# Kernel tuning notes

Measured on AMD Instinct MI355X. Metric: run time of the kernel, lower is better.

## Reference

```python
import jax, jax.numpy as jnp
import numpy as np

# Constants mirroring privacy_config
LEAK = 0.95          # membrane_leak_rate
REFR = 2.0           # refractory_period
SYN_EPS = 0.1        # synaptic_epsilon (threshold noise scale & privacy-cost factor)
NOISE_SCALE = 0.05   # spike_noise_scale on inputs
THRESH = 1.0         # spike_threshold init
SIZES = [1024, 2048, 1024, 512]
T, B = 16, 256


def setup_inputs() -> dict:
    key = jax.random.key(0)
    ks = jax.random.split(key, 16)
    inp = {"inputs": jax.random.normal(ks[0], (B, SIZES[0]), dtype=jnp.float32)}
    for i in range(3):
        nin, nout = SIZES[i], SIZES[i + 1]
        inp[f"w{i}"] = jax.random.normal(ks[1 + i], (nout, nin), dtype=jnp.float32) * 0.1
        inp[f"th{i}"] = jnp.full((nout,), THRESH, dtype=jnp.float32)
        inp[f"cn{i}"] = jax.random.normal(ks[4 + i], (T, B, nout), dtype=jnp.float32)
        inp[f"tn{i}"] = jax.random.normal(ks[7 + i], (T, B, nout), dtype=jnp.float32)
    inp["time_steps"] = T
    return inp


def _forward(inputs, ws, ths, cns, tns):
    # Vectorized leaky integrate-and-fire across (batch, neuron), scanned over time.
    Bsz = inputs.shape[0]
    Tn = cns[0].shape[0]
    nL = len(ws)
    V0 = tuple(jnp.zeros((Bsz, w.shape[0]), inputs.dtype) for w in ws)
    ls0 = tuple(jnp.full((Bsz, w.shape[0]), -1e9, inputs.dtype) for w in ws)  # last spike time
    wnorms = [jnp.linalg.norm(w, axis=1) for w in ws]  # per-neuron weight-vector norm [N]
    times = jnp.arange(1, Tn + 1, dtype=inputs.dtype)

    def step(carry, xs):
        t, cn_t, tn_t = xs
        Vs, ls = carry
        act = inputs  # input is re-presented at each time step (layer_activities[0])
        nV, nls, sps = [], [], []
        for i in range(nL):
            # per-neuron input noise ~ N(0, scale^2) dotted with w -> N(0, scale^2*||w||^2)
            cur = act @ ws[i].T + cn_t[i] * (NOISE_SCALE * wnorms[i])  # [B, N]
            refrac = (t - ls[i]) < REFR  # refractory neurons skip the update entirely
            Vn = jnp.where(refrac, Vs[i], LEAK * Vs[i] + cur)
            thr = ths[i] + tn_t[i] * SYN_EPS  # noisy privacy threshold
            sp = jnp.logical_and(jnp.logical_not(refrac), Vn > thr)
            nV.append(jnp.where(sp, 0.0, Vn))         # reset membrane on spike
            nls.append(jnp.where(sp, t, ls[i]))
            act = sp.astype(inputs.dtype)              # spikes feed next layer
            sps.append(act)
        return (tuple(nV), tuple(nls)), tuple(sps)

    _, spikes = jax.lax.scan(step, (V0, ls0), (times, tuple(cns), tuple(tns)))
    # spikes: tuple of [T, B, N_l] per layer

    # privacy cost: eps * (spikes in trailing 10-step window)/10 * ||w_neuron||, summed over all calls
    idx = jnp.arange(Tn)
    idx_hi = idx + 1
    idx_lo = jnp.clip(idx - 9, 0, Tn)
    cost = jnp.zeros((), inputs.dtype)
    tot = jnp.zeros((), inputs.dtype)
    cnt = 0
    for sp, wn in zip(spikes, wnorms):
        cs = jnp.concatenate([jnp.zeros_like(sp[:1]), jnp.cumsum(sp, axis=0)], axis=0)
        win = cs[idx_hi] - cs[idx_lo]  # [T, B, N] trailing-window spike counts
        cost = cost + SYN_EPS * jnp.sum(win / 10.0 * wn)
        tot = tot + jnp.sum(sp)
        cnt += sp.size
    # network entropy over the binary {0,1} spike pattern values
    p1 = tot / cnt
    p0 = 1.0 - p1
    eps = 1e-12
    entropy = -(p1 * jnp.log2(p1 + eps) + p0 * jnp.log2(p0 + eps))

    out = spikes[-1][-1]  # last layer activity at final time step, [B, N_last]
    return out, cost, entropy


def reference(inputs, w0, w1, w2, th0, th1, th2, cn0, cn1, cn2, tn0, tn1, tn2, time_steps):
    return _forward(inputs, (w0, w1, w2), (th0, th1, th2), (cn0, cn1, cn2), (tn0, tn1, tn2))
```

## Files before the change

### kernel.cpp

```cpp
#include <hip/hip_runtime.h>
#include <math.h>


#define T_STEPS 16

typedef short short8 __attribute__((ext_vector_type(8)));
typedef float floatx4 __attribute__((ext_vector_type(4)));

__device__ inline ushort f2bf(float x) {
  unsigned int u = __float_as_uint(x);
  unsigned int r = (u + 0x7FFFu + ((u >> 16) & 1u)) >> 16;
  return (ushort)r;
}
__device__ inline float bf2f(ushort h) {
  return __uint_as_float(((unsigned int)h) << 16);
}
__device__ inline floatx4 mfma16(short8 a, short8 b, floatx4 c) {
  return __builtin_amdgcn_mfma_f32_16x16x32_bf16(a, b, c, 0, 0, 0);
}

__device__ inline void gload16(const ushort* g, ushort* l) {
  __builtin_amdgcn_global_load_lds(
      (const __attribute__((address_space(1))) void*)g,
      (__attribute__((address_space(3))) void*)l, 16, 0, 0);
}

__device__ inline void stage_split16(const float* __restrict__ src, ushort* dsth, ushort* dstl) {
  float fv[16];
  #pragma unroll
  for (int i = 0; i < 4; ++i) *(float4*)&fv[4 * i] = *(const float4*)(src + 4 * i);
  unsigned int ph[8], pl[8];
  #pragma unroll
  for (int i = 0; i < 8; ++i) {
    ushort h0 = f2bf(fv[2 * i]);
    ushort l0 = f2bf(fv[2 * i] - bf2f(h0));
    ushort h1 = f2bf(fv[2 * i + 1]);
    ushort l1 = f2bf(fv[2 * i + 1] - bf2f(h1));
    ph[i] = (unsigned int)h0 | ((unsigned int)h1 << 16);
    pl[i] = (unsigned int)l0 | ((unsigned int)l1 << 16);
  }
  *(uint4*)dsth       = make_uint4(ph[0], ph[1], ph[2], ph[3]);
  *(uint4*)(dsth + 8) = make_uint4(ph[4], ph[5], ph[6], ph[7]);
  *(uint4*)dstl       = make_uint4(pl[0], pl[1], pl[2], pl[3]);
  *(uint4*)(dstl + 8) = make_uint4(pl[4], pl[5], pl[6], pl[7]);
}

__device__ inline void cost_store_bucket(float csum, int cnt, float2* __restrict__ cbuf,
                                         int bucket_base) {
  #pragma unroll
  for (int off = 32; off > 0; off >>= 1) {
    csum += __shfl_down(csum, off);
    cnt  += __shfl_down(cnt, off);
  }
  __shared__ float sc[4];
  __shared__ int   si[4];
  int wid = threadIdx.x >> 6;
  if ((threadIdx.x & 63) == 0) { sc[wid] = csum; si[wid] = cnt; }
  __syncthreads();
  if (threadIdx.x == 0) {
    float c = sc[0] + sc[1] + sc[2] + sc[3];
    int   k = si[0] + si[1] + si[2] + si[3];
    float2 v;
    v.x = c * 0.01f;
    v.y = (float)k;
    cbuf[bucket_base + blockIdx.x] = v;
  }
}


__global__ __launch_bounds__(256) void setup_kernel(const float* __restrict__ w0,
                                                    const float* __restrict__ w1,
                                                    const float* __restrict__ w2,
                                                    const float* __restrict__ inputs,
                                                    float* __restrict__ wn,
                                                    ushort* __restrict__ w1b,
                                                    ushort* __restrict__ w2b,
                                                    float* __restrict__ base0C) {
  __shared__ ushort Ah[64][72], Al[64][72], Bh[64][72], Bl[64][72];
  const int bid = blockIdx.x;
  const int tid = threadIdx.x;

  if (bid < 896) {
    int r = bid * 4 + (tid >> 6);
    int lane = tid & 63;
    const float* row; int K;
    if (r < 2048)      { row = w0 + (size_t)r * 1024;          K = 1024; }
    else if (r < 3072) { row = w1 + (size_t)(r - 2048) * 2048; K = 2048; }
    else               { row = w2 + (size_t)(r - 3072) * 1024; K = 1024; }
    float ss = 0.f;
    for (int k = lane; k < K; k += 64) { float x = row[k]; ss += x * x; }
    #pragma unroll
    for (int off = 32; off > 0; off >>= 1) ss += __shfl_down(ss, off);
    if (lane == 0) wn[r] = sqrtf(ss);
    return;
  }
  if (bid < 2176) {
    int i = ((bid - 896) * 256 + tid) * 8;
    const float* src; ushort* dst;
    if (i < 2097152) { src = w1 + i; dst = w1b + i; }
    else             { src = w2 + (i - 2097152); dst = w2b + (i - 2097152); }
    float4 a = *(const float4*)src;
    float4 b = *(const float4*)(src + 4);
    unsigned int p0 = (unsigned int)f2bf(a.x) | ((unsigned int)f2bf(a.y) << 16);
    unsigned int p1 = (unsigned int)f2bf(a.z) | ((unsigned int)f2bf(a.w) << 16);
    unsigned int p2 = (unsigned int)f2bf(b.x) | ((unsigned int)f2bf(b.y) << 16);
    unsigned int p3 = (unsigned int)f2bf(b.z) | ((unsigned int)f2bf(b.w) << 16);
    *(uint4*)dst = make_uint4(p0, p1, p2, p3);
    return;
  }

  const int rb = bid - 2176;
  const int m0 = (rb & 3) * 64;
  const int n0 = (rb >> 2) * 64;
  const int lane = tid & 63, wv = tid >> 6;
  const int wm = wv & 1, wn2 = wv >> 1;
  const int l15 = lane & 15, quad = lane >> 4;
  const int sr = tid >> 2, scol = (tid & 3) * 16;

  floatx4 acc[2][2];
  #pragma unroll
  for (int i = 0; i < 2; ++i)
    #pragma unroll
    for (int j = 0; j < 2; ++j) acc[i][j] = (floatx4){0.f, 0.f, 0.f, 0.f};

  for (int k0 = 0; k0 < 1024; k0 += 64) {
    stage_split16(inputs + (size_t)(m0 + sr) * 1024 + k0 + scol, &Ah[sr][scol], &Al[sr][scol]);
    stage_split16(w0 + (size_t)(n0 + sr) * 1024 + k0 + scol, &Bh[sr][scol], &Bl[sr][scol]);
    __syncthreads();
    #pragma unroll
    for (int ks = 0; ks < 2; ++ks) {
      short8 ah[2], al[2], bh[2], bl[2];
      #pragma unroll
      for (int s = 0; s < 2; ++s) {
        ah[s] = *(const short8*)&Ah[32 * wm + 16 * s + l15][ks * 32 + quad * 8];
        al[s] = *(const short8*)&Al[32 * wm + 16 * s + l15][ks * 32 + quad * 8];
        bh[s] = *(const short8*)&Bh[32 * wn2 + 16 * s + l15][ks * 32 + quad * 8];
        bl[s] = *(const short8*)&Bl[32 * wn2 + 16 * s + l15][ks * 32 + quad * 8];
      }
      #pragma unroll
      for (int sm = 0; sm < 2; ++sm)
        #pragma unroll
        for (int sn = 0; sn < 2; ++sn) {
          acc[sm][sn] = mfma16(ah[sm], bh[sn], acc[sm][sn]);
          acc[sm][sn] = mfma16(ah[sm], bl[sn], acc[sm][sn]);
          acc[sm][sn] = mfma16(al[sm], bh[sn], acc[sm][sn]);
        }
    }
    __syncthreads();
  }
  #pragma unroll
  for (int sm = 0; sm < 2; ++sm)
    #pragma unroll
    for (int sn = 0; sn < 2; ++sn)
      #pragma unroll
      for (int r = 0; r < 4; ++r) {
        int m = m0 + 32 * wm + 16 * sm + quad * 4 + r;
        int n = n0 + 32 * wn2 + 16 * sn + l15;
        base0C[(size_t)m * 2048 + n] = acc[sm][sn][r];
      }
}


template<int K, int N, int BM, bool LAST>
__global__ __launch_bounds__(256) void gemm_lif_kernel(const ushort* __restrict__ A,
                                                       const ushort* __restrict__ W,
                                                       const float* __restrict__ cn,
                                                       const float* __restrict__ tn,
                                                       const float* __restrict__ th,
                                                       const float* __restrict__ wnv,
                                                       ushort* __restrict__ spout,
                                                       float* __restrict__ outF,
                                                       float2* __restrict__ cbuf,
                                                       int bucket_base) {
  __shared__ __attribute__((aligned(16))) ushort As[2][BM * 64];
  __shared__ __attribute__((aligned(16))) ushort Bs[2][64 * 64];
  constexpr int NSTEP = K / 64;
  constexpr int NT = N / 64;
  constexpr int MT = 4096 / BM;
  constexpr int NWG = MT * NT;
  constexpr int SM = BM / 32;

  const int orig = ((int)blockIdx.x % 8) * (NWG / 8) + (int)blockIdx.x / 8;
  const int m0 = (orig / NT) * BM;
  const int n0 = (orig % NT) * 64;

  const int tid = threadIdx.x;
  const int lane = tid & 63, wv = tid >> 6;
  const int wm = wv & 1, wn2 = wv >> 1;
  const int l15 = lane & 15, quad = lane >> 4;

  const ushort* Ab = A + (size_t)m0 * K;
  const ushort* Wb = W + (size_t)n0 * K;

  const int lrow = lane >> 3;
  const int lslot = (lane & 7) ^ lrow;

  floatx4 acc[SM][2];
  #pragma unroll
  for (int i = 0; i < SM; ++i)
    #pragma unroll
    for (int j = 0; j < 2; ++j) acc[i][j] = (floatx4){0.f, 0.f, 0.f, 0.f};

  auto stage = [&](int buf, int k0) {
    #pragma unroll
    for (int h = 0; h < SM; ++h) {
      int r0 = wv * (BM / 4) + h * 8;
      gload16(Ab + (size_t)(r0 + lrow) * K + k0 + lslot * 8, &As[buf][r0 * 64]);
    }
    #pragma unroll
    for (int h = 0; h < 2; ++h) {
      int r0 = wv * 16 + h * 8;
      gload16(Wb + (size_t)(r0 + lrow) * K + k0 + lslot * 8, &Bs[buf][r0 * 64]);
    }
  };
  auto compute = [&](int buf) {
    #pragma unroll
    for (int ks = 0; ks < 2; ++ks) {
      short8 af[SM], bf[2];
      #pragma unroll
      for (int s = 0; s < SM; ++s) {
        int arow = wm * (BM / 2) + s * 16 + l15;
        af[s] = *(const short8*)&As[buf][arow * 64 + (((ks * 4 + quad) ^ (arow & 7)) << 3)];
      }
      #pragma unroll
      for (int s = 0; s < 2; ++s) {
        int brow = wn2 * 32 + s * 16 + l15;
        bf[s] = *(const short8*)&Bs[buf][brow * 64 + (((ks * 4 + quad) ^ (brow & 7)) << 3)];
      }
      #pragma unroll
      for (int sm = 0; sm < SM; ++sm)
        #pragma unroll
        for (int sn = 0; sn < 2; ++sn)
          acc[sm][sn] = mfma16(af[sm], bf[sn], acc[sm][sn]);
    }
  };

  stage(0, 0);
  __syncthreads();
  for (int kk = 0; kk < NSTEP; ++kk) {
    int buf = kk & 1;
    if (kk + 1 < NSTEP) stage(buf ^ 1, (kk + 1) * 64);
    compute(buf);
    __syncthreads();
  }

  float csum = 0.f; int cnt = 0;
  #pragma unroll
  for (int sm = 0; sm < SM; ++sm) {
    const int b = (m0 >> 4) + wm * SM + sm;
    #pragma unroll
    for (int sn = 0; sn < 2; ++sn) {
      const int n = n0 + wn2 * 32 + sn * 16 + l15;
      float cnv[4], tnv[4];
      #pragma unroll
      for (int r = 0; r < 4; ++r) {
        size_t off = (size_t)(quad * 4 + r) * (256 * N) + (size_t)b * N + n;
        cnv[r] = cn[off];
        tnv[r] = tn[off];
      }
      const float thn = th[n];
      const float wnn = wnv[n];
      float V = 0.f; int prev = 0;
      ushort skeep[4] = {0, 0, 0, 0};
      #pragma unroll
      for (int qq = 0; qq < 4; ++qq) {
        float Vl = V; int pl = prev;
        ushort slocal[4];
        #pragma unroll
        for (int r = 0; r < 4; ++r) {
          float cur = acc[sm][sn][r] + cnv[r] * (0.05f * wnn);
          float Vn = pl ? Vl : (0.95f * Vl + cur);
          float thr = thn + tnv[r] * 0.1f;
          bool sp = (!pl) && (Vn > thr);
          Vl = sp ? 0.f : Vn;
          slocal[r] = sp ? (ushort)0x3F80 : (ushort)0;
          pl = sp ? 1 : 0;
        }
        if (quad == qq) {
          #pragma unroll
          for (int r = 0; r < 4; ++r) skeep[r] = slocal[r];
        }
        V = __shfl(Vl, l15 + (qq << 4));
        prev = __shfl(pl, l15 + (qq << 4));
      }
      #pragma unroll
      for (int r = 0; r < 4; ++r) {
        int t = quad * 4 + r + 1;
        float f = (t <= 7) ? 10.f : (float)(17 - t);
        if (skeep[r]) { csum += wnn * f; cnt++; }
      }
      if (!LAST) {
        const int mbase = m0 + wm * (BM / 2) + sm * 16 + quad * 4;
        #pragma unroll
        for (int r = 0; r < 4; ++r)
          spout[(size_t)(mbase + r) * N + n] = skeep[r];
      } else {
        if (quad == 3) outF[(size_t)b * N + n] = skeep[3] ? 1.f : 0.f;
      }
    }
  }
  cost_store_bucket(csum, cnt, cbuf, bucket_base);
}


__global__ __launch_bounds__(256) void l0_lif_kernel(const float* __restrict__ base0,
                                                     const float* __restrict__ cn0,
                                                     const float* __restrict__ tn0,
                                                     const float* __restrict__ th0,
                                                     const float* __restrict__ wn0,
                                                     ushort* __restrict__ sp0,
                                                     float2* __restrict__ cbuf) {
  const int e = (blockIdx.x * 256 + threadIdx.x) * 4;
  const int n = e & 2047;
  const int b = e >> 11;
  float4 bb  = *(const float4*)(base0 + e);
  float4 th4 = *(const float4*)(th0 + n);
  float4 wn4 = *(const float4*)(wn0 + n);
  float bbv[4] = {bb.x, bb.y, bb.z, bb.w};
  float thv[4] = {th4.x, th4.y, th4.z, th4.w};
  float wnq[4] = {wn4.x, wn4.y, wn4.z, wn4.w};
  float V[4] = {0.f, 0.f, 0.f, 0.f};
  bool prev[4] = {false, false, false, false};
  float csum = 0.f; int cnt = 0;
  #pragma unroll 2
  for (int t = 1; t <= T_STEPS; ++t) {
    size_t off = (size_t)(t - 1) * 524288 + e;
    float4 c4 = *(const float4*)(cn0 + off);
    float4 t4 = *(const float4*)(tn0 + off);
    float cnv[4] = {c4.x, c4.y, c4.z, c4.w};
    float tnv[4] = {t4.x, t4.y, t4.z, t4.w};
    float f = (t <= 7) ? 10.f : (float)(17 - t);
    ushort sout[4];
    #pragma unroll
    for (int j = 0; j < 4; ++j) {
      float cur = bbv[j] + cnv[j] * (0.05f * wnq[j]);
      float Vn = prev[j] ? V[j] : (0.95f * V[j] + cur);
      float thr = thv[j] + tnv[j] * 0.1f;
      bool sp = (!prev[j]) && (Vn > thr);
      V[j] = sp ? 0.f : Vn;
      sout[j] = sp ? (ushort)0x3F80 : (ushort)0;
      prev[j] = sp;
      if (sp) { csum += wnq[j] * f; cnt++; }
    }
    ushort4 sq; sq.x = sout[0]; sq.y = sout[1]; sq.z = sout[2]; sq.w = sout[3];
    *(ushort4*)(sp0 + (size_t)(b * 16 + t - 1) * 2048 + n) = sq;
  }
  cost_store_bucket(csum, cnt, cbuf, 0);
}


__global__ __launch_bounds__(256) void finalize_kernel(const float2* __restrict__ cbuf,
                                                       float* __restrict__ out) {
  float c = 0.f, k = 0.f;
  for (int i = threadIdx.x; i < 1536; i += 256) {
    float2 v = cbuf[i];
    c += v.x; k += v.y;
  }
  #pragma unroll
  for (int off = 32; off > 0; off >>= 1) {
    c += __shfl_down(c, off);
    k += __shfl_down(k, off);
  }
  __shared__ float sc[4], sk[4];
  int wid = threadIdx.x >> 6;
  if ((threadIdx.x & 63) == 0) { sc[wid] = c; sk[wid] = k; }
  __syncthreads();
  if (threadIdx.x == 0) {
    float cost = sc[0] + sc[1] + sc[2] + sc[3];
    float tot  = sk[0] + sk[1] + sk[2] + sk[3];
    float p1 = tot / 14680064.f;
    float p0 = 1.f - p1;
    float ent = -(p1 * log2f(p1 + 1e-12f) + p0 * log2f(p0 + 1e-12f));
    out[131072] = cost;
    out[131073] = ent;
  }
}


extern "C" void kernel_launch(void* const* d_in, const int* in_sizes, int n_in,
                              void* d_out, int out_size, void* d_ws, size_t ws_size,
                              hipStream_t stream) {
  const float* inputs = (const float*)d_in[0];
  const float* w0  = (const float*)d_in[1];
  const float* th0 = (const float*)d_in[2];
  const float* cn0 = (const float*)d_in[3];
  const float* tn0 = (const float*)d_in[4];
  const float* w1  = (const float*)d_in[5];
  const float* th1 = (const float*)d_in[6];
  const float* cn1 = (const float*)d_in[7];
  const float* tn1 = (const float*)d_in[8];
  const float* w2  = (const float*)d_in[9];
  const float* th2 = (const float*)d_in[10];
  const float* cn2 = (const float*)d_in[11];
  const float* tn2 = (const float*)d_in[12];
  float* out = (float*)d_out;
  float* ws  = (float*)d_ws;

  float* wn    = ws;
  float* base0 = ws + 4096;
  ushort* w1b  = (ushort*)(base0 + 524288);
  ushort* w2b  = w1b + 2097152;
  ushort* sp0  = w2b + 524288;
  ushort* sp1  = sp0 + 8388608;
  float2* cbuf = (float2*)(sp1 + 4194304);

  setup_kernel<<<2304, 256, 0, stream>>>(w0, w1, w2, inputs, wn, w1b, w2b, base0);

  l0_lif_kernel<<<512, 256, 0, stream>>>(base0, cn0, tn0, th0, wn, sp0, cbuf);

  gemm_lif_kernel<2048, 1024, 128, false><<<512, 256, 0, stream>>>(
      sp0, w1b, cn1, tn1, th1, wn + 2048, sp1, nullptr, cbuf, 512);

  gemm_lif_kernel<1024, 512, 64, true><<<512, 256, 0, stream>>>(
      sp1, w2b, cn2, tn2, th2, wn + 3072, nullptr, out, cbuf, 1024);

  finalize_kernel<<<1, 256, 0, stream>>>(cbuf, out);
}
```

Measured before the change: 280.3 us.

## Split layer-0 GEMM over K into four slices and reduce partials in LIF kernel

The layer-0 input GEMM inside setup_kernel is split along K into four slices of 256, so 512 blocks run it instead of 128 and each block has a shorter serial K loop. Each slice writes its own partial-sum buffer, and the layer-0 LIF kernel adds the four partials when it loads the base current. GEMM blocks are also moved to the lowest block indices so they are scheduled first, ahead of the norm and conversion blocks. In exchange there is extra workspace and more global-memory traffic, and the different summation order slightly changes fp32 rounding, which could flip spikes that sit near the threshold.

```diff
diff --git a/kernel.cpp b/kernel.cpp
--- a/kernel.cpp
+++ b/kernel.cpp
@@ -75,27 +75,13 @@
                                                     float* __restrict__ wn,
                                                     ushort* __restrict__ w1b,
                                                     ushort* __restrict__ w2b,
-                                                    float* __restrict__ base0C) {
+                                                    float* __restrict__ P0) {
   __shared__ ushort Ah[64][72], Al[64][72], Bh[64][72], Bl[64][72];
   const int bid = blockIdx.x;
   const int tid = threadIdx.x;
 
-  if (bid < 896) {
-    int r = bid * 4 + (tid >> 6);
-    int lane = tid & 63;
-    const float* row; int K;
-    if (r < 2048)      { row = w0 + (size_t)r * 1024;          K = 1024; }
-    else if (r < 3072) { row = w1 + (size_t)(r - 2048) * 2048; K = 2048; }
-    else               { row = w2 + (size_t)(r - 3072) * 1024; K = 1024; }
-    float ss = 0.f;
-    for (int k = lane; k < K; k += 64) { float x = row[k]; ss += x * x; }
-    #pragma unroll
-    for (int off = 32; off > 0; off >>= 1) ss += __shfl_down(ss, off);
-    if (lane == 0) wn[r] = sqrtf(ss);
-    return;
-  }
-  if (bid < 2176) {
-    int i = ((bid - 896) * 256 + tid) * 8;
+  if (bid >= 1408) {
+    int i = ((bid - 1408) * 256 + tid) * 8;
     const float* src; ushort* dst;
     if (i < 2097152) { src = w1 + i; dst = w1b + i; }
     else             { src = w2 + (i - 2097152); dst = w2b + (i - 2097152); }
@@ -108,10 +94,25 @@
     *(uint4*)dst = make_uint4(p0, p1, p2, p3);
     return;
   }
-
-  const int rb = bid - 2176;
-  const int m0 = (rb & 3) * 64;
-  const int n0 = (rb >> 2) * 64;
+  if (bid >= 512) {
+    int r = (bid - 512) * 4 + (tid >> 6);
+    int lane = tid & 63;
+    const float* row; int K;
+    if (r < 2048)      { row = w0 + (size_t)r * 1024;          K = 1024; }
+    else if (r < 3072) { row = w1 + (size_t)(r - 2048) * 2048; K = 2048; }
+    else               { row = w2 + (size_t)(r - 3072) * 1024; K = 1024; }
+    float ss = 0.f;
+    for (int k = lane; k < K; k += 64) { float x = row[k]; ss += x * x; }
+    #pragma unroll
+    for (int off = 32; off > 0; off >>= 1) ss += __shfl_down(ss, off);
+    if (lane == 0) wn[r] = sqrtf(ss);
+    return;
+  }
+
+  const int m0 = (bid & 3) * 64;
+  const int n0 = ((bid >> 2) & 31) * 64;
+  const int sl = bid >> 7;
+  const int kbase = sl * 256;
   const int lane = tid & 63, wv = tid >> 6;
   const int wm = wv & 1, wn2 = wv >> 1;
   const int l15 = lane & 15, quad = lane >> 4;
@@ -123,9 +124,9 @@
     #pragma unroll
     for (int j = 0; j < 2; ++j) acc[i][j] = (floatx4){0.f, 0.f, 0.f, 0.f};
 
-  for (int k0 = 0; k0 < 1024; k0 += 64) {
-    stage_split16(inputs + (size_t)(m0 + sr) * 1024 + k0 + scol, &Ah[sr][scol], &Al[sr][scol]);
-    stage_split16(w0 + (size_t)(n0 + sr) * 1024 + k0 + scol, &Bh[sr][scol], &Bl[sr][scol]);
+  for (int k0 = 0; k0 < 256; k0 += 64) {
+    stage_split16(inputs + (size_t)(m0 + sr) * 1024 + kbase + k0 + scol, &Ah[sr][scol], &Al[sr][scol]);
+    stage_split16(w0 + (size_t)(n0 + sr) * 1024 + kbase + k0 + scol, &Bh[sr][scol], &Bl[sr][scol]);
     __syncthreads();
     #pragma unroll
     for (int ks = 0; ks < 2; ++ks) {
@@ -148,6 +149,7 @@
     }
     __syncthreads();
   }
+  float* Ps = P0 + (size_t)sl * 524288;
   #pragma unroll
   for (int sm = 0; sm < 2; ++sm)
     #pragma unroll
@@ -156,7 +158,7 @@
       for (int r = 0; r < 4; ++r) {
         int m = m0 + 32 * wm + 16 * sm + quad * 4 + r;
         int n = n0 + 32 * wn2 + 16 * sn + l15;
-        base0C[(size_t)m * 2048 + n] = acc[sm][sn][r];
+        Ps[(size_t)m * 2048 + n] = acc[sm][sn][r];
       }
 }
 
@@ -303,7 +305,7 @@
 }
 
 
-__global__ __launch_bounds__(256) void l0_lif_kernel(const float* __restrict__ base0,
+__global__ __launch_bounds__(256) void l0_lif_kernel(const float* __restrict__ P0,
                                                      const float* __restrict__ cn0,
                                                      const float* __restrict__ tn0,
                                                      const float* __restrict__ th0,
@@ -313,10 +315,14 @@
   const int e = (blockIdx.x * 256 + threadIdx.x) * 4;
   const int n = e & 2047;
   const int b = e >> 11;
-  float4 bb  = *(const float4*)(base0 + e);
+  float4 b0 = *(const float4*)(P0 + e);
+  float4 b1 = *(const float4*)(P0 + 524288 + e);
+  float4 b2 = *(const float4*)(P0 + 1048576 + e);
+  float4 b3 = *(const float4*)(P0 + 1572864 + e);
   float4 th4 = *(const float4*)(th0 + n);
   float4 wn4 = *(const float4*)(wn0 + n);
-  float bbv[4] = {bb.x, bb.y, bb.z, bb.w};
+  float bbv[4] = {b0.x + b1.x + b2.x + b3.x, b0.y + b1.y + b2.y + b3.y,
+                  b0.z + b1.z + b2.z + b3.z, b0.w + b1.w + b2.w + b3.w};
   float thv[4] = {th4.x, th4.y, th4.z, th4.w};
   float wnq[4] = {wn4.x, wn4.y, wn4.z, wn4.w};
   float V[4] = {0.f, 0.f, 0.f, 0.f};
@@ -397,16 +403,16 @@
   float* ws  = (float*)d_ws;
 
   float* wn    = ws;
-  float* base0 = ws + 4096;
-  ushort* w1b  = (ushort*)(base0 + 524288);
+  float* P0    = ws + 4096;
+  ushort* w1b  = (ushort*)(P0 + 2097152);
   ushort* w2b  = w1b + 2097152;
   ushort* sp0  = w2b + 524288;
   ushort* sp1  = sp0 + 8388608;
   float2* cbuf = (float2*)(sp1 + 4194304);
 
-  setup_kernel<<<2304, 256, 0, stream>>>(w0, w1, w2, inputs, wn, w1b, w2b, base0);
-
-  l0_lif_kernel<<<512, 256, 0, stream>>>(base0, cn0, tn0, th0, wn, sp0, cbuf);
+  setup_kernel<<<2688, 256, 0, stream>>>(w0, w1, w2, inputs, wn, w1b, w2b, P0);
+
+  l0_lif_kernel<<<512, 256, 0, stream>>>(P0, cn0, tn0, th0, wn, sp0, cbuf);
 
   gemm_lif_kernel<2048, 1024, 128, false><<<512, 256, 0, stream>>>(
       sp0, w1b, cn1, tn1, th1, wn + 2048, sp1, nullptr, cbuf, 512);
```

Measured after the change: 258.6 us. 1.08x faster.
